# Performance work log

Hardware: AMD Instinct MI355X
Metric: run time of the kernel (lower is better)

Reference implementation:

```python
import jax, jax.numpy as jnp
import numpy as np

OUT_DIM = 4096
IN_DIM = 4096
N_NNZ = 1600000
BATCH = 8192


def setup_inputs() -> dict:
    key = jax.random.key(0)
    k1, k2, k3 = jax.random.split(key, 3)
    x = jax.random.normal(k1, (BATCH, IN_DIM), dtype=jnp.float32)
    # COO indices of the transposed kernel: (row=output idx, col=input idx)
    rows = jax.random.randint(k2, (N_NNZ, 1), 0, OUT_DIM, dtype=jnp.int64)
    cols = jax.random.randint(jax.random.fold_in(k2, 1), (N_NNZ, 1), 0, IN_DIM, dtype=jnp.int64)
    indices = jnp.concatenate([rows, cols], axis=1)  # (N_NNZ, 2)
    values = jax.random.normal(k3, (N_NNZ,), dtype=jnp.float32) * 0.02
    return {"x": x, "indices": indices, "values": values}


def reference(x, indices, values):
    # kernel_t is a sparse (OUT_DIM, IN_DIM) matrix. In JAX the efficient
    # faithful form is to scatter the nonzeros into a dense matrix (duplicate
    # indices sum, matching SpMM semantics) and do a single dense GEMM.
    rows = indices[:, 0]
    cols = indices[:, 1]
    W_t = jnp.zeros((OUT_DIM, IN_DIM), dtype=values.dtype).at[rows, cols].add(values)
    # output = (kernel_t @ x^T)^T = x @ kernel_t^T, then ReLU activation.
    out = jax.nn.relu(jnp.einsum("bi,oi->bo", x, W_t))
    return out
```

## Files before the change

### kernel.cpp

```cpp
#include <hip/hip_runtime.h>
#include <hip/hip_bf16.h>
#include <stdint.h>

#define M_DIM 8192
#define N_DIM 4096
#define K_DIM 4096
#define NNZ   1600000

typedef __attribute__((ext_vector_type(8))) short bf16x8;
typedef __attribute__((ext_vector_type(4))) float f32x4;

static const size_t WF32_OFF  = 0;
static const size_t WBF16_OFF = 64ull << 20;
static const size_t XB_OFF    = 96ull << 20;
static const size_t WS_NEED   = 160ull << 20;

__device__ __forceinline__ unsigned short f2bf(float f) {
    union { float f; uint32_t u; } a; a.f = f;
    uint32_t u = a.u;
    uint32_t r = (u + 0x7FFFu + ((u >> 16) & 1u)) >> 16;
    return (unsigned short)r;
}

__global__ void scatter_kernel(const int* __restrict__ idx,
                               const float* __restrict__ vals,
                               float* __restrict__ W) {
    int t = blockIdx.x * blockDim.x + threadIdx.x;
    if (t < NNZ) {
        int2 rc = ((const int2*)idx)[t];
        atomicAdd(&W[(size_t)rc.x * K_DIM + rc.y], vals[t]);
    }
}

__global__ void f32_to_bf16_kernel(const float* __restrict__ src,
                                   unsigned short* __restrict__ dst, int n4) {
    int t = blockIdx.x * blockDim.x + threadIdx.x;
    if (t < n4) {
        float4 v = ((const float4*)src)[t];
        ushort4 o;
        o.x = f2bf(v.x); o.y = f2bf(v.y); o.z = f2bf(v.z); o.w = f2bf(v.w);
        ((ushort4*)dst)[t] = o;
    }
}

#define GLOAD16(gp, lp) __builtin_amdgcn_global_load_lds( \
    (const __attribute__((address_space(1))) void*)(gp),  \
    (__attribute__((address_space(3))) void*)(lp), 16, 0, 0)
#define VMCNT(n)   asm volatile("s_waitcnt vmcnt(" #n ")" ::: "memory")
#define LGKMCNT(n) asm volatile("s_waitcnt lgkmcnt(" #n ")" ::: "memory")
#define BAR() __builtin_amdgcn_s_barrier()
#define SCHED0() __builtin_amdgcn_sched_barrier(0)

#define FRAG(T, r, kk) \
    (*(const bf16x8*)&(T)[(r)*64 + (((((kk)<<2) + l4) ^ ((r)&7)) << 3)])

#define STAGE_A(buf, kt, h) do {                                              \
    GLOAD16(Ab + (size_t)((h)*128 + rl0) * K_DIM + (kt) + cs0,                \
            &sA[buf][(h)*8192 + wid*512]);                                    \
    GLOAD16(Ab + (size_t)((h)*128 + rl1) * K_DIM + (kt) + cs1,                \
            &sA[buf][(h)*8192 + 4096 + wid*512]);                             \
  } while (0)
#define STAGE_B(buf, kt, h) do {                                              \
    GLOAD16(Bb + (size_t)((h)*128 + rl0) * K_DIM + (kt) + cs0,                \
            &sB[buf][(h)*8192 + wid*512]);                                    \
    GLOAD16(Bb + (size_t)((h)*128 + rl1) * K_DIM + (kt) + cs1,                \
            &sB[buf][(h)*8192 + 4096 + wid*512]);                             \
  } while (0)

__global__ __launch_bounds__(512, 2) void gemm256_8ph(
        const __hip_bfloat16* __restrict__ A,
        const __hip_bfloat16* __restrict__ B,
        float* __restrict__ C)
{
    __shared__ __align__(16) __hip_bfloat16 sA[2][256 * 64];
    __shared__ __align__(16) __hip_bfloat16 sB[2][256 * 64];

    const int tid  = threadIdx.x;
    const int lane = tid & 63;
    const int wid  = tid >> 6;
    const int wr   = wid >> 2;
    const int wc   = wid & 3;
    const int l15  = lane & 15, l4 = lane >> 4;

    const int bid = blockIdx.x;
    const int swz = (bid & 7) * 64 + (bid >> 3);
    const int m0  = (swz >> 4) * 256;
    const int n0  = (swz & 15) * 256;

    const int s0 = tid, s1 = 512 + tid;
    const int rl0 = s0 >> 3, cs0 = ((s0 & 7) ^ (rl0 & 7)) << 3;
    const int rl1 = s1 >> 3, cs1 = ((s1 & 7) ^ (rl1 & 7)) << 3;
    const __hip_bfloat16* Ab = A + (size_t)m0 * K_DIM;
    const __hip_bfloat16* Bb = B + (size_t)n0 * K_DIM;

    f32x4  acc[8][4] = {};
    bf16x8 aLo[4][2], aHi[4][2], bLo[2][2], bHi[2][2];

    STAGE_A(0, 0, 0);  STAGE_A(0, 0, 1);
    STAGE_B(0, 0, 0);  STAGE_B(0, 0, 1);
    STAGE_A(1, 64, 0); STAGE_A(1, 64, 1);
    VMCNT(4);
    BAR();

    for (int t = 0; t < 64; ++t) {
        const int c = t & 1;
        const __hip_bfloat16* TA = sA[c];
        const __hip_bfloat16* TB = sB[c];
        const int ktn = (t + 1) << 6;

        #pragma unroll
        for (int m = 0; m < 4; ++m) {
            const int r = wr * 128 + m * 16 + l15;
            aLo[m][0] = FRAG(TA, r, 0);
            aLo[m][1] = FRAG(TA, r, 1);
        }
        #pragma unroll
        for (int n = 0; n < 2; ++n) {
            const int r = wc * 64 + n * 16 + l15;
            bLo[n][0] = FRAG(TB, r, 0);
            bLo[n][1] = FRAG(TB, r, 1);
        }
        if (t < 63) STAGE_B(c ^ 1, ktn, 0);
        LGKMCNT(8);
        BAR();
        LGKMCNT(0); SCHED0();
        __builtin_amdgcn_s_setprio(1);
        #pragma unroll
        for (int k = 0; k < 2; ++k)
            #pragma unroll
            for (int m = 0; m < 4; ++m)
                #pragma unroll
                for (int n = 0; n < 2; ++n)
                    acc[m][n] = __builtin_amdgcn_mfma_f32_16x16x32_bf16(
                                    aLo[m][k], bLo[n][k], acc[m][n], 0, 0, 0);
        __builtin_amdgcn_s_setprio(0);
        BAR();

        #pragma unroll
        for (int m = 0; m < 4; ++m) {
            const int r = wr * 128 + 64 + m * 16 + l15;
            aHi[m][0] = FRAG(TA, r, 0);
            aHi[m][1] = FRAG(TA, r, 1);
        }
        if (t < 63) STAGE_B(c ^ 1, ktn, 1);
        BAR();
        LGKMCNT(0); SCHED0();
        __builtin_amdgcn_s_setprio(1);
        #pragma unroll
        for (int k = 0; k < 2; ++k)
            #pragma unroll
            for (int m = 0; m < 4; ++m)
                #pragma unroll
                for (int n = 0; n < 2; ++n)
                    acc[4 + m][n] = __builtin_amdgcn_mfma_f32_16x16x32_bf16(
                                    aHi[m][k], bLo[n][k], acc[4 + m][n], 0, 0, 0);
        __builtin_amdgcn_s_setprio(0);
        BAR();

        #pragma unroll
        for (int n = 0; n < 2; ++n) {
            const int r = wc * 64 + 32 + n * 16 + l15;
            bHi[n][0] = FRAG(TB, r, 0);
            bHi[n][1] = FRAG(TB, r, 1);
        }
        BAR();
        LGKMCNT(0); SCHED0();
        __builtin_amdgcn_s_setprio(1);
        #pragma unroll
        for (int k = 0; k < 2; ++k)
            #pragma unroll
            for (int m = 0; m < 4; ++m)
                #pragma unroll
                for (int n = 0; n < 2; ++n)
                    acc[4 + m][2 + n] = __builtin_amdgcn_mfma_f32_16x16x32_bf16(
                                    aHi[m][k], bHi[n][k], acc[4 + m][2 + n], 0, 0, 0);
        __builtin_amdgcn_s_setprio(0);
        BAR();

        __builtin_amdgcn_s_setprio(1);
        #pragma unroll
        for (int k = 0; k < 2; ++k)
            #pragma unroll
            for (int m = 0; m < 4; ++m)
                #pragma unroll
                for (int n = 0; n < 2; ++n)
                    acc[m][2 + n] = __builtin_amdgcn_mfma_f32_16x16x32_bf16(
                                    aLo[m][k], bHi[n][k], acc[m][2 + n], 0, 0, 0);
        __builtin_amdgcn_s_setprio(0);

        if (t < 62) {
            STAGE_A(c, ktn + 64, 0);
            STAGE_A(c, ktn + 64, 1);
            VMCNT(4);
            BAR();
        } else if (t == 62) {
            VMCNT(0);
            BAR();
        }
    }

    const int row_base = m0 + wr * 128;
    const int col_base = n0 + wc * 64;
    #pragma unroll
    for (int mq = 0; mq < 2; ++mq)
        #pragma unroll
        for (int m = 0; m < 4; ++m)
            #pragma unroll
            for (int nq = 0; nq < 2; ++nq)
                #pragma unroll
                for (int n = 0; n < 2; ++n) {
                    const f32x4 v = acc[mq * 4 + m][nq * 2 + n];
                    const int col = col_base + nq * 32 + n * 16 + l15;
                    #pragma unroll
                    for (int j = 0; j < 4; ++j) {
                        const int row = row_base + mq * 64 + m * 16 + l4 * 4 + j;
                        C[(size_t)row * N_DIM + col] = fmaxf(v[j], 0.0f);
                    }
                }
}

__global__ void gemm_f32_fallback(const float* __restrict__ A,
                                  const float* __restrict__ W,
                                  float* __restrict__ C) {
    __shared__ float As[64][17];
    __shared__ float Bs[64][17];
    const int tx = threadIdx.x & 15, ty = threadIdx.x >> 4;
    const int m0 = blockIdx.y * 64, n0 = blockIdx.x * 64;
    float acc[4][4] = {};
    for (int kt = 0; kt < K_DIM; kt += 16) {
        #pragma unroll
        for (int i = 0; i < 4; ++i) {
            int e = threadIdx.x + i * 256;
            int r = e >> 4, k = e & 15;
            As[r][k] = A[(size_t)(m0 + r) * K_DIM + kt + k];
            Bs[r][k] = W[(size_t)(n0 + r) * K_DIM + kt + k];
        }
        __syncthreads();
        #pragma unroll
        for (int k = 0; k < 16; ++k) {
            float av[4], bv[4];
            #pragma unroll
            for (int i = 0; i < 4; ++i) av[i] = As[ty * 4 + i][k];
            #pragma unroll
            for (int i = 0; i < 4; ++i) bv[i] = Bs[tx * 4 + i][k];
            #pragma unroll
            for (int i = 0; i < 4; ++i)
                #pragma unroll
                for (int j = 0; j < 4; ++j) acc[i][j] += av[i] * bv[j];
        }
        __syncthreads();
    }
    #pragma unroll
    for (int i = 0; i < 4; ++i)
        #pragma unroll
        for (int j = 0; j < 4; ++j)
            C[(size_t)(m0 + ty * 4 + i) * N_DIM + n0 + tx * 4 + j] =
                fmaxf(acc[i][j], 0.0f);
}

extern "C" void kernel_launch(void* const* d_in, const int* in_sizes, int n_in,
                              void* d_out, int out_size, void* d_ws, size_t ws_size,
                              hipStream_t stream) {
    const float* x       = (const float*)d_in[0];
    const int*   indices = (const int*)d_in[1];
    const float* values  = (const float*)d_in[2];
    float*       out     = (float*)d_out;

    float* Wf = (float*)((char*)d_ws + WF32_OFF);

    hipMemsetAsync(Wf, 0, (size_t)N_DIM * K_DIM * sizeof(float), stream);
    scatter_kernel<<<(NNZ + 255) / 256, 256, 0, stream>>>(indices, values, Wf);

    if (ws_size >= WS_NEED) {
        unsigned short* Wb = (unsigned short*)((char*)d_ws + WBF16_OFF);
        unsigned short* xb = (unsigned short*)((char*)d_ws + XB_OFF);

        {
            int n4 = (N_DIM * K_DIM) / 4;
            f32_to_bf16_kernel<<<(n4 + 255) / 256, 256, 0, stream>>>(Wf, Wb, n4);
        }
        {
            int n4 = (M_DIM * K_DIM) / 4;
            f32_to_bf16_kernel<<<(n4 + 255) / 256, 256, 0, stream>>>(x, xb, n4);
        }

        gemm256_8ph<<<(M_DIM / 256) * (N_DIM / 256), 512, 0, stream>>>(
            (const __hip_bfloat16*)xb, (const __hip_bfloat16*)Wb, out);
    } else {
        gemm_f32_fallback<<<dim3(N_DIM / 64, M_DIM / 64), 256, 0, stream>>>(
            x, Wf, out);
    }
}
```

Before: 417.0 us.

## Restructure GEMM prefetch schedule with per-group staging and fewer barriers

Rewrites the software pipeline of the bf16 MFMA GEMM so that A and B tiles are staged in 64-row groups. Loads for the next B stage and for the stage after next are spread across the four MFMA phases. It drops the explicit LDS waitcnt and sched_barrier fences and removes several block barriers per iteration. It also unrolls the K loop by two. The aim is to overlap global-to-LDS traffic with compute and cut synchronisation stalls. The cost is that correctness now leans on compiler-inserted waits, which makes LDS buffer reuse more fragile.

```diff
diff --git a/kernel.cpp b/kernel.cpp
--- a/kernel.cpp
+++ b/kernel.cpp
@@ -47,27 +47,19 @@
     (const __attribute__((address_space(1))) void*)(gp),  \
     (__attribute__((address_space(3))) void*)(lp), 16, 0, 0)
 #define VMCNT(n)   asm volatile("s_waitcnt vmcnt(" #n ")" ::: "memory")
-#define LGKMCNT(n) asm volatile("s_waitcnt lgkmcnt(" #n ")" ::: "memory")
-#define BAR() __builtin_amdgcn_s_barrier()
-#define SCHED0() __builtin_amdgcn_sched_barrier(0)
+#define BAR()    __builtin_amdgcn_s_barrier()
 
 #define FRAG(T, r, kk) \
-    (*(const bf16x8*)&(T)[(r)*64 + (((((kk)<<2) + l4) ^ ((r)&7)) << 3)])
-
-#define STAGE_A(buf, kt, h) do {                                              \
-    GLOAD16(Ab + (size_t)((h)*128 + rl0) * K_DIM + (kt) + cs0,                \
-            &sA[buf][(h)*8192 + wid*512]);                                    \
-    GLOAD16(Ab + (size_t)((h)*128 + rl1) * K_DIM + (kt) + cs1,                \
-            &sA[buf][(h)*8192 + 4096 + wid*512]);                             \
-  } while (0)
-#define STAGE_B(buf, kt, h) do {                                              \
-    GLOAD16(Bb + (size_t)((h)*128 + rl0) * K_DIM + (kt) + cs0,                \
-            &sB[buf][(h)*8192 + wid*512]);                                    \
-    GLOAD16(Bb + (size_t)((h)*128 + rl1) * K_DIM + (kt) + cs1,                \
-            &sB[buf][(h)*8192 + 4096 + wid*512]);                             \
-  } while (0)
-
-__global__ __launch_bounds__(512, 2) void gemm256_8ph(
+    (*(const bf16x8*)&(T)[(r) * 64 + (((((kk) << 2) + l4) ^ ((r) & 7)) << 3)])
+
+#define STAGE_AG(buf, tt, g) \
+    GLOAD16(Ab + (size_t)((g) * 64 + rbase) * K_DIM + (size_t)(tt) * 64 + cs, \
+            &sA[buf][(g) * 4096 + wid * 512])
+#define STAGE_BG(buf, tt, g) \
+    GLOAD16(Bb + (size_t)((g) * 64 + rbase) * K_DIM + (size_t)(tt) * 64 + cs, \
+            &sB[buf][(g) * 4096 + wid * 512])
+
+__global__ __launch_bounds__(512, 2) void gemm256_v5(
         const __hip_bfloat16* __restrict__ A,
         const __hip_bfloat16* __restrict__ B,
         float* __restrict__ C)
@@ -87,26 +79,29 @@
     const int m0  = (swz >> 4) * 256;
     const int n0  = (swz & 15) * 256;
 
-    const int s0 = tid, s1 = 512 + tid;
-    const int rl0 = s0 >> 3, cs0 = ((s0 & 7) ^ (rl0 & 7)) << 3;
-    const int rl1 = s1 >> 3, cs1 = ((s1 & 7) ^ (rl1 & 7)) << 3;
+    const int rbase = tid >> 3;
+    const int cs    = ((tid & 7) ^ (rbase & 7)) << 3;
+
     const __hip_bfloat16* Ab = A + (size_t)m0 * K_DIM;
     const __hip_bfloat16* Bb = B + (size_t)n0 * K_DIM;
 
-    f32x4  acc[8][4] = {};
-    bf16x8 aLo[4][2], aHi[4][2], bLo[2][2], bHi[2][2];
-
-    STAGE_A(0, 0, 0);  STAGE_A(0, 0, 1);
-    STAGE_B(0, 0, 0);  STAGE_B(0, 0, 1);
-    STAGE_A(1, 64, 0); STAGE_A(1, 64, 1);
-    VMCNT(4);
+    f32x4 acc[8][4] = {};
+
+    STAGE_AG(0, 0, 0); STAGE_AG(0, 0, 1); STAGE_AG(0, 0, 2); STAGE_AG(0, 0, 3);
+    STAGE_BG(0, 0, 0); STAGE_BG(0, 0, 1); STAGE_BG(0, 0, 2); STAGE_BG(0, 0, 3);
+    STAGE_AG(1, 1, 0); STAGE_AG(1, 1, 1); STAGE_AG(1, 1, 2); STAGE_AG(1, 1, 3);
+    STAGE_BG(1, 1, 0); STAGE_BG(1, 1, 1);
+    VMCNT(6);
     BAR();
 
-    for (int t = 0; t < 64; ++t) {
+    const int NT = K_DIM / 64;
+    #pragma unroll 2
+    for (int t = 0; t < NT; ++t) {
         const int c = t & 1;
         const __hip_bfloat16* TA = sA[c];
         const __hip_bfloat16* TB = sB[c];
-        const int ktn = (t + 1) << 6;
+
+        bf16x8 aLo[4][2], aHi[4][2], bLo[2][2], bHi[2][2];
 
         #pragma unroll
         for (int m = 0; m < 4; ++m) {
@@ -120,10 +115,7 @@
             bLo[n][0] = FRAG(TB, r, 0);
             bLo[n][1] = FRAG(TB, r, 1);
         }
-        if (t < 63) STAGE_B(c ^ 1, ktn, 0);
-        LGKMCNT(8);
-        BAR();
-        LGKMCNT(0); SCHED0();
+        BAR();
         __builtin_amdgcn_s_setprio(1);
         #pragma unroll
         for (int k = 0; k < 2; ++k)
@@ -134,7 +126,7 @@
                     acc[m][n] = __builtin_amdgcn_mfma_f32_16x16x32_bf16(
                                     aLo[m][k], bLo[n][k], acc[m][n], 0, 0, 0);
         __builtin_amdgcn_s_setprio(0);
-        BAR();
+        if (t + 1 < NT) { STAGE_BG(c ^ 1, t + 1, 2); STAGE_BG(c ^ 1, t + 1, 3); }
 
         #pragma unroll
         for (int m = 0; m < 4; ++m) {
@@ -142,9 +134,7 @@
             aHi[m][0] = FRAG(TA, r, 0);
             aHi[m][1] = FRAG(TA, r, 1);
         }
-        if (t < 63) STAGE_B(c ^ 1, ktn, 1);
-        BAR();
-        LGKMCNT(0); SCHED0();
+        BAR();
         __builtin_amdgcn_s_setprio(1);
         #pragma unroll
         for (int k = 0; k < 2; ++k)
@@ -155,7 +145,6 @@
                     acc[4 + m][n] = __builtin_amdgcn_mfma_f32_16x16x32_bf16(
                                     aHi[m][k], bLo[n][k], acc[4 + m][n], 0, 0, 0);
         __builtin_amdgcn_s_setprio(0);
-        BAR();
 
         #pragma unroll
         for (int n = 0; n < 2; ++n) {
@@ -164,7 +153,6 @@
             bHi[n][1] = FRAG(TB, r, 1);
         }
         BAR();
-        LGKMCNT(0); SCHED0();
         __builtin_amdgcn_s_setprio(1);
         #pragma unroll
         for (int k = 0; k < 2; ++k)
@@ -175,8 +163,12 @@
                     acc[4 + m][2 + n] = __builtin_amdgcn_mfma_f32_16x16x32_bf16(
                                     aHi[m][k], bHi[n][k], acc[4 + m][2 + n], 0, 0, 0);
         __builtin_amdgcn_s_setprio(0);
-        BAR();
-
+        if (t + 2 < NT) {
+            STAGE_AG(c, t + 2, 0); STAGE_AG(c, t + 2, 1);
+            STAGE_AG(c, t + 2, 2); STAGE_AG(c, t + 2, 3);
+        }
+
+        BAR();
         __builtin_amdgcn_s_setprio(1);
         #pragma unroll
         for (int k = 0; k < 2; ++k)
@@ -187,13 +179,12 @@
                     acc[m][2 + n] = __builtin_amdgcn_mfma_f32_16x16x32_bf16(
                                     aLo[m][k], bHi[n][k], acc[m][2 + n], 0, 0, 0);
         __builtin_amdgcn_s_setprio(0);
-
-        if (t < 62) {
-            STAGE_A(c, ktn + 64, 0);
-            STAGE_A(c, ktn + 64, 1);
-            VMCNT(4);
+        if (t + 2 < NT) { STAGE_BG(c, t + 2, 0); STAGE_BG(c, t + 2, 1); }
+
+        if (t < NT - 2) {
+            VMCNT(6);
             BAR();
-        } else if (t == 62) {
+        } else if (t == NT - 2) {
             VMCNT(0);
             BAR();
         }
@@ -202,21 +193,17 @@
     const int row_base = m0 + wr * 128;
     const int col_base = n0 + wc * 64;
     #pragma unroll
-    for (int mq = 0; mq < 2; ++mq)
-        #pragma unroll
-        for (int m = 0; m < 4; ++m)
-            #pragma unroll
-            for (int nq = 0; nq < 2; ++nq)
-                #pragma unroll
-                for (int n = 0; n < 2; ++n) {
-                    const f32x4 v = acc[mq * 4 + m][nq * 2 + n];
-                    const int col = col_base + nq * 32 + n * 16 + l15;
-                    #pragma unroll
-                    for (int j = 0; j < 4; ++j) {
-                        const int row = row_base + mq * 64 + m * 16 + l4 * 4 + j;
-                        C[(size_t)row * N_DIM + col] = fmaxf(v[j], 0.0f);
-                    }
-                }
+    for (int m = 0; m < 8; ++m)
+        #pragma unroll
+        for (int n = 0; n < 4; ++n) {
+            const f32x4 v = acc[m][n];
+            const int col = col_base + n * 16 + l15;
+            #pragma unroll
+            for (int j = 0; j < 4; ++j) {
+                const int row = row_base + m * 16 + l4 * 4 + j;
+                C[(size_t)row * N_DIM + col] = fmaxf(v[j], 0.0f);
+            }
+        }
 }
 
 __global__ void gemm_f32_fallback(const float* __restrict__ A,
@@ -284,7 +271,7 @@
             f32_to_bf16_kernel<<<(n4 + 255) / 256, 256, 0, stream>>>(x, xb, n4);
         }
 
-        gemm256_8ph<<<(M_DIM / 256) * (N_DIM / 256), 512, 0, stream>>>(
+        gemm256_v5<<<(M_DIM / 256) * (N_DIM / 256), 512, 0, stream>>>(
             (const __hip_bfloat16*)xb, (const __hip_bfloat16*)Wb, out);
     } else {
         gemm_f32_fallback<<<dim3(N_DIM / 64, M_DIM / 64), 256, 0, stream>>>(
```

Result: faster. 362.3 us (-13.1%).
